# Kernel tuning notes

Hardware: AMD Instinct MI355X
Metric: run time of the kernel (lower is better)

## Reference

```python
import jax, jax.numpy as jnp
import numpy as np

EMBED_DIM = 1024
NUM_HEADS = 16
HEAD_DIM = EMBED_DIM // NUM_HEADS
ROPE_THETA = 10000.0


def setup_inputs() -> dict:
    key = jax.random.key(0)
    k1, k2, k3, k4, k5 = jax.random.split(key, 5)
    B, S, E = 2, 2048, EMBED_DIM
    scale = 1.0 / np.sqrt(E)
    x = jax.random.normal(k1, (B, S, E), dtype=jnp.float32)
    w_qkv = jax.random.normal(k2, (E, 3 * E), dtype=jnp.float32) * scale
    b_qkv = jnp.zeros((3 * E,), dtype=jnp.float32)
    w_o = jax.random.normal(k3, (E, E), dtype=jnp.float32) * scale
    b_o = jnp.zeros((E,), dtype=jnp.float32)
    return {"x": x, "w_qkv": w_qkv, "b_qkv": b_qkv, "w_o": w_o, "b_o": b_o}


def _rope_cos_sin(seq_len, dtype):
    # half-dim frequencies, GPT-NeoX rotate-half convention
    inv_freq = 1.0 / (ROPE_THETA ** (jnp.arange(0, HEAD_DIM, 2, dtype=jnp.float32) / HEAD_DIM))
    pos = jnp.arange(seq_len, dtype=jnp.float32)
    freqs = pos[:, None] * inv_freq[None, :]          # [S, hd/2]
    emb = jnp.concatenate([freqs, freqs], axis=-1)    # [S, hd]
    return jnp.cos(emb).astype(dtype), jnp.sin(emb).astype(dtype)


def _rotate_half(t):
    t1, t2 = jnp.split(t, 2, axis=-1)
    return jnp.concatenate([-t2, t1], axis=-1)


def reference(x, w_qkv, b_qkv, w_o, b_o):
    B, S, E = x.shape
    H, D = NUM_HEADS, HEAD_DIM
    qkv = x @ w_qkv + b_qkv                            # [B, S, 3E]
    q, k, v = jnp.split(qkv, 3, axis=-1)
    # [B, H, S, D]
    q = q.reshape(B, S, H, D).transpose(0, 2, 1, 3)
    k = k.reshape(B, S, H, D).transpose(0, 2, 1, 3)
    v = v.reshape(B, S, H, D).transpose(0, 2, 1, 3)
    cos, sin = _rope_cos_sin(S, x.dtype)               # [S, D]
    q = q * cos + _rotate_half(q) * sin
    k = k * cos + _rotate_half(k) * sin
    scores = jnp.einsum('bhqd,bhkd->bhqk', q, k) / jnp.sqrt(jnp.asarray(D, x.dtype))
    causal = jnp.tril(jnp.ones((S, S), dtype=bool))
    scores = jnp.where(causal, scores, jnp.asarray(-1e30, x.dtype))
    attn = jax.nn.softmax(scores, axis=-1)
    out = jnp.einsum('bhqk,bhkd->bhqd', attn, v)       # [B, H, S, D]
    out = out.transpose(0, 2, 1, 3).reshape(B, S, E)
    return out @ w_o + b_o
```

## Files before the change

kernel.cpp:

```cpp
#include <hip/hip_runtime.h>
#include <hip/hip_bf16.h>

typedef __hip_bfloat16 bf16_t;
typedef __attribute__((ext_vector_type(8))) __bf16 bf16x8;
typedef __attribute__((ext_vector_type(4))) float f32x4;
typedef __attribute__((ext_vector_type(4))) unsigned short ushort4v;
typedef __attribute__((ext_vector_type(4))) short short4v;

#define NUM_B 2
#define NUM_H 16
#define SEQ   2048
#define EMB   1024
#define LOG2E 1.44269504088896340736f
#define LN10K 13.287712379549449f

__global__ __launch_bounds__(256) void prep_kernel(
    const float* __restrict__ x, const float* __restrict__ wq,
    const float* __restrict__ wo, bf16_t* __restrict__ xb,
    bf16_t* __restrict__ wqT, bf16_t* __restrict__ woT) {
  __shared__ float tile[32][33];
  int bid = blockIdx.x, tid = threadIdx.x;
  if (bid < 4096) {
    int i = (bid * 256 + tid) * 4;
    f32x4 v = *(const f32x4*)&x[i];
    ushort4v p;
#pragma unroll
    for (int j = 0; j < 4; ++j)
      p[j] = __builtin_bit_cast(unsigned short, __float2bfloat16(v[j]));
    *(ushort4v*)&xb[i] = p;
    return;
  }
  const float* src;
  bf16_t* dst;
  int R, C, c0, r0;
  if (bid < 4096 + 3072) {
    int b = bid - 4096;
    src = wq; dst = wqT; R = 1024; C = 3072;
    c0 = (b % 96) * 32; r0 = (b / 96) * 32;
  } else {
    int b = bid - 7168;
    src = wo; dst = woT; R = 1024; C = 1024;
    c0 = (b % 32) * 32; r0 = (b / 32) * 32;
  }
  int tx = tid & 31, ty = tid >> 5;
#pragma unroll
  for (int i = 0; i < 4; ++i)
    tile[ty + i * 8][tx] = src[(size_t)(r0 + ty + i * 8) * C + c0 + tx];
  __syncthreads();
#pragma unroll
  for (int i = 0; i < 4; ++i)
    dst[(size_t)(c0 + ty + i * 8) * R + r0 + tx] = __float2bfloat16(tile[tx][ty + i * 8]);
}

template <int CH>
__device__ __forceinline__ void stage_tile(const bf16_t* __restrict__ G,
                                           int row0, int col0, int ld,
                                           bf16_t* Ls, int tid) {
#pragma unroll
  for (int r = 0; r < CH; ++r) {
    int c = tid + r * 256;
    int row = c >> 2, g = c & 3;
    const char* gp = (const char*)(G + (size_t)(row0 + row) * ld + col0) +
                     ((g ^ ((row >> 1) & 3)) * 16);
    char* lp = (char*)Ls + c * 16;
    __builtin_amdgcn_global_load_lds((const __attribute__((address_space(1))) void*)gp,
                                     (__attribute__((address_space(3))) void*)lp, 16, 0, 0);
  }
}

template <int MODE, int MT>
__global__ __launch_bounds__(256) void gemm_bf16_kernel(
    const bf16_t* __restrict__ A, const bf16_t* __restrict__ Bt,
    const float* __restrict__ bias, bf16_t* __restrict__ out0,
    bf16_t* __restrict__ out1, bf16_t* __restrict__ out2,
    float* __restrict__ outf, int Ndim, int Kdim) {
  __shared__ __align__(16) bf16_t As[MT * 32 * 32];
  __shared__ __align__(16) bf16_t Bs[128 * 32];
  int tid = threadIdx.x;
  int wave = tid >> 6, lane = tid & 63;
  int lr = lane & 15, lq = lane >> 4;
  int m0 = blockIdx.x * (32 * MT), n0 = blockIdx.y * 128;
  int wm = (wave >> 1) * (MT * 16), wn = (wave & 1) * 64;
  int key = (lr >> 1) & 3;
  int goff = ((lq ^ key) * 8);
  f32x4 acc[MT][4];
#pragma unroll
  for (int i = 0; i < MT; ++i)
#pragma unroll
    for (int j = 0; j < 4; ++j) acc[i][j] = (f32x4){0.f, 0.f, 0.f, 0.f};

  for (int k0 = 0; k0 < Kdim; k0 += 32) {
    __syncthreads();
    stage_tile<MT / 2>(A, m0, k0, Kdim, As, tid);
    stage_tile<2>(Bt, n0, k0, Kdim, Bs, tid);
    __syncthreads();
    bf16x8 af[MT], bfr[4];
#pragma unroll
    for (int mt = 0; mt < MT; ++mt)
      af[mt] = *(const bf16x8*)&As[(wm + mt * 16 + lr) * 32 + goff];
#pragma unroll
    for (int nt = 0; nt < 4; ++nt)
      bfr[nt] = *(const bf16x8*)&Bs[(wn + nt * 16 + lr) * 32 + goff];
#pragma unroll
    for (int mt = 0; mt < MT; ++mt)
#pragma unroll
      for (int nt = 0; nt < 4; ++nt)
        acc[mt][nt] = __builtin_amdgcn_mfma_f32_16x16x32_bf16(af[mt], bfr[nt], acc[mt][nt], 0, 0, 0);
  }

  if (MODE == 0) {
#pragma unroll
    for (int pr = 0; pr < 2; ++pr) {
      int na = n0 + wn + pr * 16 + lr;
      int nb = na + 32;
      int sec = na >> 10;
      int h = (na >> 6) & (NUM_H - 1);
      int da = na & 63;
      float bva = bias[na], bvb = bias[nb];
      if (sec == 2) {
#pragma unroll
        for (int mt = 0; mt < MT; ++mt) {
          int mbase = m0 + wm + mt * 16 + lq * 4;
          int b = mbase >> 11;
          int s = mbase & (SEQ - 1);
          int bh = b * NUM_H + h;
          ushort4v pa, pb;
#pragma unroll
          for (int r = 0; r < 4; ++r) {
            pa[r] = __builtin_bit_cast(unsigned short, __float2bfloat16(acc[mt][pr][r] + bva));
            pb[r] = __builtin_bit_cast(unsigned short, __float2bfloat16(acc[mt][pr + 2][r] + bvb));
          }
          *(ushort4v*)&out2[((size_t)bh * 64 + da) * SEQ + s] = pa;
          *(ushort4v*)&out2[((size_t)bh * 64 + da + 32) * SEQ + s] = pb;
        }
      } else {
        bf16_t* dst = (sec == 0) ? out0 : out1;
        float scale = (sec == 0) ? 0.125f : 1.0f;
        int i = da & 31;
        float inv = exp2f(-(float)i * (LN10K / 32.0f));
        float c1, s1;
        sincosf(inv, &s1, &c1);
#pragma unroll
        for (int mt = 0; mt < MT; ++mt) {
          int mbase = m0 + wm + mt * 16 + lq * 4;
          int b = mbase >> 11;
          int s0 = mbase & (SEQ - 1);
          int bh = b * NUM_H + h;
          float sn, cs;
          sincosf((float)s0 * inv, &sn, &cs);
#pragma unroll
          for (int r = 0; r < 4; ++r) {
            float va = acc[mt][pr][r] + bva;
            float vb = acc[mt][pr + 2][r] + bvb;
            float oa = (va * cs - vb * sn) * scale;
            float ob = (vb * cs + va * sn) * scale;
            size_t rowb = ((size_t)bh * SEQ + (s0 + r)) * 64;
            dst[rowb + da] = __float2bfloat16(oa);
            dst[rowb + da + 32] = __float2bfloat16(ob);
            float csn = cs * c1 - sn * s1;
            sn = sn * c1 + cs * s1;
            cs = csn;
          }
        }
      }
    }
  } else {
#pragma unroll
    for (int nt = 0; nt < 4; ++nt) {
      int n = n0 + wn + nt * 16 + lr;
      float bv = bias[n];
#pragma unroll
      for (int mt = 0; mt < MT; ++mt)
#pragma unroll
        for (int r = 0; r < 4; ++r) {
          int m = m0 + wm + mt * 16 + lq * 4 + r;
          outf[(size_t)m * Ndim + n] = acc[mt][nt][r] + bv;
        }
    }
  }
}

__device__ __forceinline__ void stage_sw(const char* __restrict__ gbase,
                                         size_t rowStride, bf16_t* lds, int tid) {
#pragma unroll
  for (int r = 0; r < 2; ++r) {
    int c = tid + r * 256;
    int row = c >> 3, g = c & 7;
    const char* gp = gbase + (size_t)row * rowStride + ((g ^ (row & 7)) * 16);
    char* lp = (char*)lds + c * 16;
    __builtin_amdgcn_global_load_lds((const __attribute__((address_space(1))) void*)gp,
                                     (__attribute__((address_space(3))) void*)lp, 16, 0, 0);
  }
}

__global__ __launch_bounds__(256) void flash_attn_kernel(
    const bf16_t* __restrict__ Q, const bf16_t* __restrict__ K,
    const bf16_t* __restrict__ Vt, bf16_t* __restrict__ O) {
  __shared__ __align__(16) bf16_t Ks[2][64 * 64];
  __shared__ __align__(16) bf16_t Vs[2][64 * 64];
  int tid = threadIdx.x;
  int wv = tid >> 6, lane = tid & 63;
  int lr = lane & 15, lq = lane >> 4;
  int bx = blockIdx.x;
  int bh = bx & 31;
  int tile = 31 - (bx >> 5);
  int qw0 = tile * 64 + wv * 16;
  const bf16_t* Qb = Q + (size_t)bh * SEQ * 64;
  const bf16_t* Kb = K + (size_t)bh * SEQ * 64;
  const bf16_t* Vb = Vt + (size_t)bh * 64 * SEQ;
  int sw = lr & 7;
  int g0 = (lq ^ sw) * 8;
  int g1 = g0 ^ 32;

  bf16x8 aq0 = *(const bf16x8*)&Qb[(size_t)(qw0 + lr) * 64 + lq * 8];
  bf16x8 aq1 = *(const bf16x8*)&Qb[(size_t)(qw0 + lr) * 64 + 32 + lq * 8];

  f32x4 Oacc[4];
#pragma unroll
  for (int dt = 0; dt < 4; ++dt) Oacc[dt] = (f32x4){0.f, 0.f, 0.f, 0.f};
  float lrow = 0.f;

  int nch = tile + 1;
  stage_sw((const char*)Kb, 128, Ks[0], tid);
  stage_sw((const char*)Vb, SEQ * 2, Vs[0], tid);

  for (int ch = 0; ch < nch; ++ch) {
    int cur = ch & 1;
    bool diag = (ch == tile);
    __syncthreads();
    if (ch + 1 < nch) {
      int kvn = (ch + 1) * 64;
      stage_sw((const char*)(Kb + (size_t)kvn * 64), 128, Ks[cur ^ 1], tid);
      stage_sw((const char*)Vb + (size_t)kvn * 2, SEQ * 2, Vs[cur ^ 1], tid);
    }

#pragma unroll
    for (int sub = 0; sub < 4; ++sub) {
      if (!diag || sub <= wv) {
        int rk = (sub * 16 + lr) * 64;
        bf16x8 k0 = *(const bf16x8*)&Ks[cur][rk + g0];
        bf16x8 k1 = *(const bf16x8*)&Ks[cur][rk + g1];
        f32x4 t = (f32x4){0.f, 0.f, 0.f, 0.f};
        t = __builtin_amdgcn_mfma_f32_16x16x32_bf16(k0, aq0, t, 0, 0, 0);
        t = __builtin_amdgcn_mfma_f32_16x16x32_bf16(k1, aq1, t, 0, 0, 0);
        if (diag && sub == wv) {
#pragma unroll
          for (int r = 0; r < 4; ++r)
            if (lq * 4 + r > lr) t[r] = -1e30f;
        }
        short4v pp;
#pragma unroll
        for (int r = 0; r < 4; ++r) {
          float p = exp2f(t[r] * LOG2E);
          lrow += p;
          pp[r] = __builtin_bit_cast(short, __float2bfloat16(p));
        }
#pragma unroll
        for (int dt = 0; dt < 4; ++dt) {
          int row = dt * 16 + lr;
          int grp = (sub * 2 + (lq >> 1)) ^ sw;
          short4v av = *(const short4v*)&Vs[cur][row * 64 + grp * 8 + (lq & 1) * 4];
          Oacc[dt] = __builtin_amdgcn_mfma_f32_16x16x16bf16_1k(av, pp, Oacc[dt], 0, 0, 0);
        }
      }
    }
  }

  lrow += __shfl_xor(lrow, 16, 64);
  lrow += __shfl_xor(lrow, 32, 64);

  int b = bh >> 4, h = bh & (NUM_H - 1);
  int q = qw0 + lr;
  size_t base = (((size_t)b * SEQ + q) * NUM_H + h) * 64;
  float rinv = 1.0f / lrow;
#pragma unroll
  for (int dt = 0; dt < 4; ++dt) {
    ushort4v ok;
#pragma unroll
    for (int r = 0; r < 4; ++r)
      ok[r] = __builtin_bit_cast(unsigned short, __float2bfloat16(Oacc[dt][r] * rinv));
    *(ushort4v*)&O[base + dt * 16 + lq * 4] = ok;
  }
}

extern "C" void kernel_launch(void* const* d_in, const int* in_sizes, int n_in,
                              void* d_out, int out_size, void* d_ws, size_t ws_size,
                              hipStream_t stream) {
  const float* x      = (const float*)d_in[0];
  const float* w_qkv  = (const float*)d_in[1];
  const float* b_qkv  = (const float*)d_in[2];
  const float* w_o    = (const float*)d_in[3];
  const float* b_o    = (const float*)d_in[4];
  float* out = (float*)d_out;

  bf16_t* ws    = (bf16_t*)d_ws;
  bf16_t* xb    = ws;
  bf16_t* wqkvT = xb + 4 * 1024 * 1024;
  bf16_t* woT   = wqkvT + 3072 * 1024;
  bf16_t* Qb    = woT + 1024 * 1024;
  bf16_t* Kb    = Qb + 4 * 1024 * 1024;
  bf16_t* Vt    = Kb + 4 * 1024 * 1024;
  bf16_t* attn  = Vt + 4 * 1024 * 1024;

  prep_kernel<<<8192, 256, 0, stream>>>(x, w_qkv, w_o, xb, wqkvT, woT);
  gemm_bf16_kernel<0, 4><<<dim3(32, 24), 256, 0, stream>>>(
      xb, wqkvT, b_qkv, Qb, Kb, Vt, nullptr, 3072, 1024);
  flash_attn_kernel<<<1024, 256, 0, stream>>>(Qb, Kb, Vt, attn);
  gemm_bf16_kernel<1, 2><<<dim3(64, 8), 256, 0, stream>>>(
      attn, woT, b_o, nullptr, nullptr, nullptr, out, 1024, 1024);
}
```

Measured before the change: 183.1 us.

## Double flash-attention KV chunk to 128 keys and fold log2e into Q scale

The flash-attention loop now stages 128 keys per chunk instead of 64. K and V LDS tiles double in size, and the swizzled staging helpers and causal diagonal-chunk logic (`dch`, `dlim`) are adjusted to match. This halves the number of `__syncthreads` barriers and loop iterations per query tile, at the cost of more LDS per block, which may limit occupancy. Separately, log2(e) is folded into the Q scaling in the QKV epilogue, so the softmax exponent skips one multiply per score.

```diff
diff --git a/kernel.cpp b/kernel.cpp
--- a/kernel.cpp
+++ b/kernel.cpp
@@ -135,7 +135,7 @@
         }
       } else {
         bf16_t* dst = (sec == 0) ? out0 : out1;
-        float scale = (sec == 0) ? 0.125f : 1.0f;
+        float scale = (sec == 0) ? 0.125f * LOG2E : 1.0f;
         int i = da & 31;
         float inv = exp2f(-(float)i * (LN10K / 32.0f));
         float c1, s1;
@@ -180,24 +180,37 @@
   }
 }
 
-__device__ __forceinline__ void stage_sw(const char* __restrict__ gbase,
-                                         size_t rowStride, bf16_t* lds, int tid) {
-#pragma unroll
-  for (int r = 0; r < 2; ++r) {
+__device__ __forceinline__ void stage_k128(const char* __restrict__ gbase,
+                                           bf16_t* lds, int tid) {
+#pragma unroll
+  for (int r = 0; r < 4; ++r) {
     int c = tid + r * 256;
     int row = c >> 3, g = c & 7;
-    const char* gp = gbase + (size_t)row * rowStride + ((g ^ (row & 7)) * 16);
+    const char* gp = gbase + (size_t)row * 128 + ((g ^ (row & 7)) * 16);
     char* lp = (char*)lds + c * 16;
     __builtin_amdgcn_global_load_lds((const __attribute__((address_space(1))) void*)gp,
                                      (__attribute__((address_space(3))) void*)lp, 16, 0, 0);
   }
 }
 
+__device__ __forceinline__ void stage_v128(const char* __restrict__ gbase,
+                                           bf16_t* lds, int tid) {
+#pragma unroll
+  for (int r = 0; r < 4; ++r) {
+    int c = tid + r * 256;
+    int row = c >> 4, g = c & 15;
+    const char* gp = gbase + (size_t)row * (SEQ * 2) + ((g ^ (row & 7)) * 16);
+    char* lp = (char*)lds + c * 16;
+    __builtin_amdgcn_global_load_lds((const __attribute__((address_space(1))) void*)gp,
+                                     (__attribute__((address_space(3))) void*)lp, 16, 0, 0);
+  }
+}
+
 __global__ __launch_bounds__(256) void flash_attn_kernel(
     const bf16_t* __restrict__ Q, const bf16_t* __restrict__ K,
     const bf16_t* __restrict__ Vt, bf16_t* __restrict__ O) {
-  __shared__ __align__(16) bf16_t Ks[2][64 * 64];
-  __shared__ __align__(16) bf16_t Vs[2][64 * 64];
+  __shared__ __align__(16) bf16_t Ks[2][128 * 64];
+  __shared__ __align__(16) bf16_t Vs[2][64 * 128];
   int tid = threadIdx.x;
   int wv = tid >> 6, lane = tid & 63;
   int lr = lane & 15, lq = lane >> 4;
@@ -220,30 +233,33 @@
   for (int dt = 0; dt < 4; ++dt) Oacc[dt] = (f32x4){0.f, 0.f, 0.f, 0.f};
   float lrow = 0.f;
 
-  int nch = tile + 1;
-  stage_sw((const char*)Kb, 128, Ks[0], tid);
-  stage_sw((const char*)Vb, SEQ * 2, Vs[0], tid);
+  int nch = (tile >> 1) + 1;
+  int dch = tile >> 1;
+  int dlim = ((tile & 1) << 2) + wv;
+
+  stage_k128((const char*)Kb, Ks[0], tid);
+  stage_v128((const char*)Vb, Vs[0], tid);
 
   for (int ch = 0; ch < nch; ++ch) {
     int cur = ch & 1;
-    bool diag = (ch == tile);
+    bool diag = (ch == dch);
     __syncthreads();
     if (ch + 1 < nch) {
-      int kvn = (ch + 1) * 64;
-      stage_sw((const char*)(Kb + (size_t)kvn * 64), 128, Ks[cur ^ 1], tid);
-      stage_sw((const char*)Vb + (size_t)kvn * 2, SEQ * 2, Vs[cur ^ 1], tid);
+      int kvn = (ch + 1) * 128;
+      stage_k128((const char*)(Kb + (size_t)kvn * 64), Ks[cur ^ 1], tid);
+      stage_v128((const char*)Vb + (size_t)kvn * 2, Vs[cur ^ 1], tid);
     }
 
 #pragma unroll
-    for (int sub = 0; sub < 4; ++sub) {
-      if (!diag || sub <= wv) {
+    for (int sub = 0; sub < 8; ++sub) {
+      if (!diag || sub <= dlim) {
         int rk = (sub * 16 + lr) * 64;
         bf16x8 k0 = *(const bf16x8*)&Ks[cur][rk + g0];
         bf16x8 k1 = *(const bf16x8*)&Ks[cur][rk + g1];
         f32x4 t = (f32x4){0.f, 0.f, 0.f, 0.f};
         t = __builtin_amdgcn_mfma_f32_16x16x32_bf16(k0, aq0, t, 0, 0, 0);
         t = __builtin_amdgcn_mfma_f32_16x16x32_bf16(k1, aq1, t, 0, 0, 0);
-        if (diag && sub == wv) {
+        if (diag && sub == dlim) {
 #pragma unroll
           for (int r = 0; r < 4; ++r)
             if (lq * 4 + r > lr) t[r] = -1e30f;
@@ -251,7 +267,7 @@
         short4v pp;
 #pragma unroll
         for (int r = 0; r < 4; ++r) {
-          float p = exp2f(t[r] * LOG2E);
+          float p = exp2f(t[r]);
           lrow += p;
           pp[r] = __builtin_bit_cast(short, __float2bfloat16(p));
         }
@@ -259,7 +275,7 @@
         for (int dt = 0; dt < 4; ++dt) {
           int row = dt * 16 + lr;
           int grp = (sub * 2 + (lq >> 1)) ^ sw;
-          short4v av = *(const short4v*)&Vs[cur][row * 64 + grp * 8 + (lq & 1) * 4];
+          short4v av = *(const short4v*)&Vs[cur][row * 128 + grp * 8 + (lq & 1) * 4];
           Oacc[dt] = __builtin_amdgcn_mfma_f32_16x16x16bf16_1k(av, pp, Oacc[dt], 0, 0, 0);
         }
       }
```

New measurement: 183.4 us. No clear change (+0.2%).

## Pair causal query tiles per block to share K/V loads and balance work

Applied to the files above, without the earlier changes.

Each attention block now handles two query tiles (tA and 31-tA) of the same head. It streams K/V chunks once and applies them to both tiles, so every block gets an equal amount of causal work and staged K/V is reused. The log2(e) factor is folded into the Q scale in the QKV GEMM epilogue, and the raw exp2 intrinsic replaces exp2f(x*LOG2E). The cost is more registers for two accumulator sets and half as many blocks, which may lower occupancy and latency hiding.

```diff
diff --git a/kernel.cpp b/kernel.cpp
--- a/kernel.cpp
+++ b/kernel.cpp
@@ -135,7 +135,7 @@
         }
       } else {
         bf16_t* dst = (sec == 0) ? out0 : out1;
-        float scale = (sec == 0) ? 0.125f : 1.0f;
+        float scale = (sec == 0) ? 0.125f * LOG2E : 1.0f;
         int i = da & 31;
         float inv = exp2f(-(float)i * (LN10K / 32.0f));
         float c1, s1;
@@ -202,9 +202,10 @@
   int wv = tid >> 6, lane = tid & 63;
   int lr = lane & 15, lq = lane >> 4;
   int bx = blockIdx.x;
-  int bh = bx & 31;
-  int tile = 31 - (bx >> 5);
-  int qw0 = tile * 64 + wv * 16;
+  int bh = bx >> 4;
+  int tA = bx & 15;
+  int tB = 31 - tA;
+  int nch = tB + 1;
   const bf16_t* Qb = Q + (size_t)bh * SEQ * 64;
   const bf16_t* Kb = K + (size_t)bh * SEQ * 64;
   const bf16_t* Vb = Vt + (size_t)bh * 64 * SEQ;
@@ -212,74 +213,107 @@
   int g0 = (lq ^ sw) * 8;
   int g1 = g0 ^ 32;
 
-  bf16x8 aq0 = *(const bf16x8*)&Qb[(size_t)(qw0 + lr) * 64 + lq * 8];
-  bf16x8 aq1 = *(const bf16x8*)&Qb[(size_t)(qw0 + lr) * 64 + 32 + lq * 8];
-
-  f32x4 Oacc[4];
-#pragma unroll
-  for (int dt = 0; dt < 4; ++dt) Oacc[dt] = (f32x4){0.f, 0.f, 0.f, 0.f};
-  float lrow = 0.f;
-
-  int nch = tile + 1;
+  int qA = tA * 64 + wv * 16, qB = tB * 64 + wv * 16;
+  bf16x8 aqA0 = *(const bf16x8*)&Qb[(size_t)(qA + lr) * 64 + lq * 8];
+  bf16x8 aqA1 = *(const bf16x8*)&Qb[(size_t)(qA + lr) * 64 + 32 + lq * 8];
+  bf16x8 aqB0 = *(const bf16x8*)&Qb[(size_t)(qB + lr) * 64 + lq * 8];
+  bf16x8 aqB1 = *(const bf16x8*)&Qb[(size_t)(qB + lr) * 64 + 32 + lq * 8];
+
+  f32x4 OA[4], OB[4];
+#pragma unroll
+  for (int dt = 0; dt < 4; ++dt) {
+    OA[dt] = (f32x4){0.f, 0.f, 0.f, 0.f};
+    OB[dt] = (f32x4){0.f, 0.f, 0.f, 0.f};
+  }
+  float lA = 0.f, lB = 0.f;
+
   stage_sw((const char*)Kb, 128, Ks[0], tid);
   stage_sw((const char*)Vb, SEQ * 2, Vs[0], tid);
 
   for (int ch = 0; ch < nch; ++ch) {
     int cur = ch & 1;
-    bool diag = (ch == tile);
     __syncthreads();
     if (ch + 1 < nch) {
       int kvn = (ch + 1) * 64;
       stage_sw((const char*)(Kb + (size_t)kvn * 64), 128, Ks[cur ^ 1], tid);
       stage_sw((const char*)Vb + (size_t)kvn * 2, SEQ * 2, Vs[cur ^ 1], tid);
     }
+    bool actA = (ch <= tA);
+    bool diagA = (ch == tA);
+    bool diagB = (ch == tB);
 
 #pragma unroll
     for (int sub = 0; sub < 4; ++sub) {
-      if (!diag || sub <= wv) {
+      bool doB = (!diagB || sub <= wv);
+      bool doA = actA && (!diagA || sub <= wv);
+      if (doB || doA) {
         int rk = (sub * 16 + lr) * 64;
         bf16x8 k0 = *(const bf16x8*)&Ks[cur][rk + g0];
         bf16x8 k1 = *(const bf16x8*)&Ks[cur][rk + g1];
-        f32x4 t = (f32x4){0.f, 0.f, 0.f, 0.f};
-        t = __builtin_amdgcn_mfma_f32_16x16x32_bf16(k0, aq0, t, 0, 0, 0);
-        t = __builtin_amdgcn_mfma_f32_16x16x32_bf16(k1, aq1, t, 0, 0, 0);
-        if (diag && sub == wv) {
-#pragma unroll
-          for (int r = 0; r < 4; ++r)
-            if (lq * 4 + r > lr) t[r] = -1e30f;
-        }
-        short4v pp;
-#pragma unroll
-        for (int r = 0; r < 4; ++r) {
-          float p = exp2f(t[r] * LOG2E);
-          lrow += p;
-          pp[r] = __builtin_bit_cast(short, __float2bfloat16(p));
+        short4v ppA, ppB;
+        if (doB) {
+          f32x4 t = (f32x4){0.f, 0.f, 0.f, 0.f};
+          t = __builtin_amdgcn_mfma_f32_16x16x32_bf16(k0, aqB0, t, 0, 0, 0);
+          t = __builtin_amdgcn_mfma_f32_16x16x32_bf16(k1, aqB1, t, 0, 0, 0);
+          if (diagB && sub == wv) {
+#pragma unroll
+            for (int r = 0; r < 4; ++r)
+              if (lq * 4 + r > lr) t[r] = -1e30f;
+          }
+#pragma unroll
+          for (int r = 0; r < 4; ++r) {
+            float p = __builtin_amdgcn_exp2f(t[r]);
+            lB += p;
+            ppB[r] = __builtin_bit_cast(short, __float2bfloat16(p));
+          }
+        }
+        if (doA) {
+          f32x4 t = (f32x4){0.f, 0.f, 0.f, 0.f};
+          t = __builtin_amdgcn_mfma_f32_16x16x32_bf16(k0, aqA0, t, 0, 0, 0);
+          t = __builtin_amdgcn_mfma_f32_16x16x32_bf16(k1, aqA1, t, 0, 0, 0);
+          if (diagA && sub == wv) {
+#pragma unroll
+            for (int r = 0; r < 4; ++r)
+              if (lq * 4 + r > lr) t[r] = -1e30f;
+          }
+#pragma unroll
+          for (int r = 0; r < 4; ++r) {
+            float p = __builtin_amdgcn_exp2f(t[r]);
+            lA += p;
+            ppA[r] = __builtin_bit_cast(short, __float2bfloat16(p));
+          }
         }
 #pragma unroll
         for (int dt = 0; dt < 4; ++dt) {
           int row = dt * 16 + lr;
           int grp = (sub * 2 + (lq >> 1)) ^ sw;
           short4v av = *(const short4v*)&Vs[cur][row * 64 + grp * 8 + (lq & 1) * 4];
-          Oacc[dt] = __builtin_amdgcn_mfma_f32_16x16x16bf16_1k(av, pp, Oacc[dt], 0, 0, 0);
+          if (doB) OB[dt] = __builtin_amdgcn_mfma_f32_16x16x16bf16_1k(av, ppB, OB[dt], 0, 0, 0);
+          if (doA) OA[dt] = __builtin_amdgcn_mfma_f32_16x16x16bf16_1k(av, ppA, OA[dt], 0, 0, 0);
         }
       }
     }
   }
 
-  lrow += __shfl_xor(lrow, 16, 64);
-  lrow += __shfl_xor(lrow, 32, 64);
+  lA += __shfl_xor(lA, 16, 64);
+  lA += __shfl_xor(lA, 32, 64);
+  lB += __shfl_xor(lB, 16, 64);
+  lB += __shfl_xor(lB, 32, 64);
 
   int b = bh >> 4, h = bh & (NUM_H - 1);
-  int q = qw0 + lr;
-  size_t base = (((size_t)b * SEQ + q) * NUM_H + h) * 64;
-  float rinv = 1.0f / lrow;
+  float rA = 1.0f / lA, rB = 1.0f / lB;
+  size_t baseA = (((size_t)b * SEQ + (qA + lr)) * NUM_H + h) * 64;
+  size_t baseB = (((size_t)b * SEQ + (qB + lr)) * NUM_H + h) * 64;
 #pragma unroll
   for (int dt = 0; dt < 4; ++dt) {
-    ushort4v ok;
-#pragma unroll
-    for (int r = 0; r < 4; ++r)
-      ok[r] = __builtin_bit_cast(unsigned short, __float2bfloat16(Oacc[dt][r] * rinv));
-    *(ushort4v*)&O[base + dt * 16 + lq * 4] = ok;
+    ushort4v oa, ob;
+#pragma unroll
+    for (int r = 0; r < 4; ++r) {
+      oa[r] = __builtin_bit_cast(unsigned short, __float2bfloat16(OA[dt][r] * rA));
+      ob[r] = __builtin_bit_cast(unsigned short, __float2bfloat16(OB[dt][r] * rB));
+    }
+    *(ushort4v*)&O[baseA + dt * 16 + lq * 4] = oa;
+    *(ushort4v*)&O[baseB + dt * 16 + lq * 4] = ob;
   }
 }
 
@@ -305,7 +339,7 @@
   prep_kernel<<<8192, 256, 0, stream>>>(x, w_qkv, w_o, xb, wqkvT, woT);
   gemm_bf16_kernel<0, 4><<<dim3(32, 24), 256, 0, stream>>>(
       xb, wqkvT, b_qkv, Qb, Kb, Vt, nullptr, 3072, 1024);
-  flash_attn_kernel<<<1024, 256, 0, stream>>>(Qb, Kb, Vt, attn);
+  flash_attn_kernel<<<512, 256, 0, stream>>>(Qb, Kb, Vt, attn);
   gemm_bf16_kernel<1, 2><<<dim3(64, 8), 256, 0, stream>>>(
       attn, woT, b_o, nullptr, nullptr, nullptr, out, 1024, 1024);
 }
```

Measured after the change: 319.4 us. 74.4% more time.
